# Performance work log

Hardware: AMD Instinct MI355X
Metric: run time of the kernel (lower is better)

The kernel has to match this reference:

```python
import jax, jax.numpy as jnp
import numpy as np

F = 50  # number of feature fields

def setup_inputs() -> dict:
    key = jax.random.key(0)
    k1, k2, k3, k4 = jax.random.split(key, 4)
    B, D, A = 4096, 16, 32
    return {
        "feat_emb": jax.random.normal(k1, (B, F, D), dtype=jnp.float32),
        "W": jax.random.normal(k2, (D, A), dtype=jnp.float32) * 0.1,
        "h": jax.random.normal(k3, (A,), dtype=jnp.float32),
        "p_vec": jax.random.normal(k4, (D,), dtype=jnp.float32),
    }

def reference(feat_emb, W, h, p_vec):
    # build_cross: upper-triangular field pairs (i < j)
    row, col = np.triu_indices(F, k=1)              # each [P], P = F*(F-1)/2
    p = feat_emb[:, row]                             # [B, P, D]
    q = feat_emb[:, col]                             # [B, P, D]
    inter = p * q                                    # pairwise interaction [B, P, D]
    # AttLayer: Dense(no bias) -> relu -> contract with h -> softmax over pairs
    att_signal = jax.nn.relu(jnp.einsum('bpd,da->bpa', inter, W))  # [B, P, A]
    scores = jnp.einsum('bpa,a->bp', att_signal, h)                # [B, P]
    att = jax.nn.softmax(scores, axis=1)                           # [B, P]
    # attention-weighted sum-pooling over pairs
    pooled = jnp.einsum('bp,bpd->bd', att, inter)                  # [B, D]
    # dropout omitted (inference); final projection and reduce
    out = jnp.einsum('bd,d->b', pooled, p_vec)[:, None]            # [B, 1]
    return out
```

## Files before the change

kernel.cpp:

```cpp
#include <hip/hip_runtime.h>
#include <math.h>


#define FF 50
#define DD 16
#define AA 32
#define NP 1225
#define NT 39
#define NTP 40
#define ERS 24
#define EBS (FF * ERS)

typedef _Float16 half8 __attribute__((ext_vector_type(8)));
typedef _Float16 half4 __attribute__((ext_vector_type(4)));
typedef _Float16 half2v __attribute__((ext_vector_type(2)));
typedef float    floatx16 __attribute__((ext_vector_type(16)));

__global__ __launch_bounds__(256, 4) void afm_kernel(
    const float* __restrict__ feat,
    const float* __restrict__ W,
    const float* __restrict__ h,
    const float* __restrict__ pvec,
    float* __restrict__ out,
    int Btot)
{
  __shared__ __align__(16) _Float16 eh[8 * EBS];
  __shared__ unsigned int tbl[NTP * 32];

  const int tid    = threadIdx.x;
  const int lane   = tid & 63;
  const int wave   = tid >> 6;
  const int halfid = lane >> 5;
  const int n      = lane & 31;
  const int b0     = blockIdx.x << 3;

  for (int s = tid; s < 8 * 200; s += 256) {
    int bl  = s / 200;
    int rem = s - bl * 200;
    int bb  = b0 + bl;
    if (bb < Btot) {
      float4 v4 = ((const float4*)feat)[(size_t)bb * 200 + rem];
      half4 hv;
      hv[0] = (_Float16)v4.x; hv[1] = (_Float16)v4.y;
      hv[2] = (_Float16)v4.z; hv[3] = (_Float16)v4.w;
      int row = rem >> 2, q = rem & 3;
      *(half4*)(&eh[bl * EBS + row * ERS + q * 4]) = hv;
    }
  }

  for (int q = tid; q < NTP * 32; q += 256) {
    int t = ((q >> 6) << 1) | (q & 1);
    int nn = (q >> 1) & 31;
    int p = t * 32 + nn;
    unsigned ent = 0;
    if (p < NP) {
      int rad = 9801 - 8 * p;
      int i = (int)((99.0f - sqrtf((float)rad)) * 0.5f);
      if (i < 0) i = 0; if (i > 48) i = 48;
      int off = (i * (99 - i)) >> 1;
      if (off > p) { --i; off = (i * (99 - i)) >> 1; }
      else {
        int off1 = ((i + 1) * (98 - i)) >> 1;
        if (off1 <= p) { ++i; off = off1; }
      }
      int j = p - off + i + 1;
      ent = ((unsigned)(i * 48) << 16) | (unsigned)(j * 48);
    }
    tbl[q] = ent;
  }

  const float LOG2E = 1.4426950408889634f;
  half8 A0;
  #pragma unroll
  for (int jj = 0; jj < 8; ++jj)
    A0[jj] = (_Float16)W[(halfid * 8 + jj) * AA + n];
  float hreg[16];
  #pragma unroll
  for (int r = 0; r < 16; ++r)
    hreg[r] = h[(r & 3) + 8 * (r >> 2) + 4 * halfid] * LOG2E;
  half8 PV;
  #pragma unroll
  for (int k = 0; k < 8; ++k) PV[k] = (_Float16)pvec[halfid * 8 + k];

  __syncthreads();

  const char* ebA = (const char*)(eh + (2 * wave) * EBS) + halfid * 16;
  const char* ebB = ebA + EBS * sizeof(_Float16);

  auto core = [&](const char* eb, unsigned oi, unsigned oj,
                  float& vout, float& gout) {
    half8 Bi = *(const half8*)(eb + oi);
    half8 Bj = *(const half8*)(eb + oj);
    half8 Bv = Bi * Bj;
    floatx16 z = __builtin_amdgcn_mfma_f32_32x32x16_f16(
        A0, Bv, (floatx16)0.0f, 0, 0, 0);
    float a0 = 0.f, a1 = 0.f, a2 = 0.f, a3 = 0.f;
    #pragma unroll
    for (int r = 0; r < 16; r += 4) {
      a0 = fmaf(fmaxf(z[r + 0], 0.f), hreg[r + 0], a0);
      a1 = fmaf(fmaxf(z[r + 1], 0.f), hreg[r + 1], a1);
      a2 = fmaf(fmaxf(z[r + 2], 0.f), hreg[r + 2], a2);
      a3 = fmaf(fmaxf(z[r + 3], 0.f), hreg[r + 3], a3);
    }
    float v = (a0 + a1) + (a2 + a3);
    vout = v + __shfl_xor(v, 32, 64);
    half8 gp = Bv * PV;
    half4 g4 = {(_Float16)(gp[0] + gp[4]), (_Float16)(gp[1] + gp[5]),
                (_Float16)(gp[2] + gp[6]), (_Float16)(gp[3] + gp[7])};
    half2v g2 = {(_Float16)(g4[0] + g4[2]), (_Float16)(g4[1] + g4[3])};
    gout = (float)g2[0] + (float)g2[1];
  };

  float denA = 0.f, numA = 0.f, denB = 0.f, numB = 0.f;

  const unsigned int* tpair = tbl + 2 * n;
  for (int th = 0; th < 19; ++th) {
    uint2 ij2 = *(const uint2*)(tpair + th * 64);
    unsigned oi0 = ij2.x >> 16, oj0 = ij2.x & 0xffffu;
    unsigned oi1 = ij2.y >> 16, oj1 = ij2.y & 0xffffu;
    float v, g;
    core(ebA, oi0, oj0, v, g);
    { float e = exp2f(v); denA += e; numA = fmaf(e, g, numA); }
    core(ebB, oi0, oj0, v, g);
    { float e = exp2f(v); denB += e; numB = fmaf(e, g, numB); }
    core(ebA, oi1, oj1, v, g);
    { float e = exp2f(v); denA += e; numA = fmaf(e, g, numA); }
    core(ebB, oi1, oj1, v, g);
    { float e = exp2f(v); denB += e; numB = fmaf(e, g, numB); }
  }
  {
    unsigned ij = tpair[19 * 64];
    unsigned oi = ij >> 16, oj = ij & 0xffffu;
    float v, g;
    core(ebA, oi, oj, v, g);
    if (n >= 9) v = -3.0e38f;
    { float e = exp2f(v); denA += e; numA = fmaf(e, g, numA); }
    core(ebB, oi, oj, v, g);
    if (n >= 9) v = -3.0e38f;
    { float e = exp2f(v); denB += e; numB = fmaf(e, g, numB); }
  }

  #pragma unroll
  for (int mask = 32; mask >= 1; mask >>= 1) {
    denA += __shfl_xor(denA, mask, 64);
    numA += __shfl_xor(numA, mask, 64);
    denB += __shfl_xor(denB, mask, 64);
    numB += __shfl_xor(numB, mask, 64);
  }
  const int bA = b0 + 2 * wave;
  if (lane == 0 && bA < Btot)     out[bA]     = (2.0f * numA) / denA;
  if (lane == 0 && bA + 1 < Btot) out[bA + 1] = (2.0f * numB) / denB;
}

extern "C" void kernel_launch(void* const* d_in, const int* in_sizes, int n_in,
                              void* d_out, int out_size, void* d_ws, size_t ws_size,
                              hipStream_t stream) {
  const float* feat = (const float*)d_in[0];
  const float* W    = (const float*)d_in[1];
  const float* h    = (const float*)d_in[2];
  const float* pvec = (const float*)d_in[3];
  float* out = (float*)d_out;
  const int B = in_sizes[0] / (FF * DD);
  afm_kernel<<<(B + 7) / 8, 256, 0, stream>>>(feat, W, h, pvec, out, B);
}
```

Before: 89.86 us.

## Process 32 samples per block with 4-sample interleaving per wave

```diff
diff --git a/kernel.cpp b/kernel.cpp
--- a/kernel.cpp
+++ b/kernel.cpp
@@ -10,13 +10,14 @@
 #define NTP 40
 #define ERS 24
 #define EBS (FF * ERS)
+#define BPB 32
 
 typedef _Float16 half8 __attribute__((ext_vector_type(8)));
 typedef _Float16 half4 __attribute__((ext_vector_type(4)));
 typedef _Float16 half2v __attribute__((ext_vector_type(2)));
 typedef float    floatx16 __attribute__((ext_vector_type(16)));
 
-__global__ __launch_bounds__(256, 4) void afm_kernel(
+__global__ __launch_bounds__(256) void afm_kernel(
     const float* __restrict__ feat,
     const float* __restrict__ W,
     const float* __restrict__ h,
@@ -24,7 +25,7 @@
     float* __restrict__ out,
     int Btot)
 {
-  __shared__ __align__(16) _Float16 eh[8 * EBS];
+  __shared__ __align__(16) _Float16 eh[BPB * EBS];
   __shared__ unsigned int tbl[NTP * 32];
 
   const int tid    = threadIdx.x;
@@ -32,9 +33,9 @@
   const int wave   = tid >> 6;
   const int halfid = lane >> 5;
   const int n      = lane & 31;
-  const int b0     = blockIdx.x << 3;
+  const int b0     = blockIdx.x * BPB;
 
-  for (int s = tid; s < 8 * 200; s += 256) {
+  for (int s = tid; s < BPB * 200; s += 256) {
     int bl  = s / 200;
     int rem = s - bl * 200;
     int bb  = b0 + bl;
@@ -81,19 +82,16 @@
   half8 PV;
   #pragma unroll
   for (int k = 0; k < 8; ++k) PV[k] = (_Float16)pvec[halfid * 8 + k];
+  const floatx16 ZACC = (floatx16)0.0f;
 
   __syncthreads();
-
-  const char* ebA = (const char*)(eh + (2 * wave) * EBS) + halfid * 16;
-  const char* ebB = ebA + EBS * sizeof(_Float16);
 
   auto core = [&](const char* eb, unsigned oi, unsigned oj,
                   float& vout, float& gout) {
     half8 Bi = *(const half8*)(eb + oi);
     half8 Bj = *(const half8*)(eb + oj);
     half8 Bv = Bi * Bj;
-    floatx16 z = __builtin_amdgcn_mfma_f32_32x32x16_f16(
-        A0, Bv, (floatx16)0.0f, 0, 0, 0);
+    floatx16 z = __builtin_amdgcn_mfma_f32_32x32x16_f16(A0, Bv, ZACC, 0, 0, 0);
     float a0 = 0.f, a1 = 0.f, a2 = 0.f, a3 = 0.f;
     #pragma unroll
     for (int r = 0; r < 16; r += 4) {
@@ -111,45 +109,61 @@
     gout = (float)g2[0] + (float)g2[1];
   };
 
-  float denA = 0.f, numA = 0.f, denB = 0.f, numB = 0.f;
+  const unsigned int* tpair = tbl + 2 * n;
 
-  const unsigned int* tpair = tbl + 2 * n;
-  for (int th = 0; th < 19; ++th) {
-    uint2 ij2 = *(const uint2*)(tpair + th * 64);
-    unsigned oi0 = ij2.x >> 16, oj0 = ij2.x & 0xffffu;
-    unsigned oi1 = ij2.y >> 16, oj1 = ij2.y & 0xffffu;
-    float v, g;
-    core(ebA, oi0, oj0, v, g);
-    { float e = exp2f(v); denA += e; numA = fmaf(e, g, numA); }
-    core(ebB, oi0, oj0, v, g);
-    { float e = exp2f(v); denB += e; numB = fmaf(e, g, numB); }
-    core(ebA, oi1, oj1, v, g);
-    { float e = exp2f(v); denA += e; numA = fmaf(e, g, numA); }
-    core(ebB, oi1, oj1, v, g);
-    { float e = exp2f(v); denB += e; numB = fmaf(e, g, numB); }
+  for (int grp = 0; grp < 2; ++grp) {
+    const int bg = b0 + wave * 8 + grp * 4;
+    const char* eb0 = (const char*)(eh + (wave * 8 + grp * 4) * EBS)
+                      + halfid * 16;
+    float den[4] = {0.f, 0.f, 0.f, 0.f};
+    float num[4] = {0.f, 0.f, 0.f, 0.f};
+
+    for (int th = 0; th < 19; ++th) {
+      uint2 ij2 = *(const uint2*)(tpair + th * 64);
+      unsigned oi0 = ij2.x >> 16, oj0 = ij2.x & 0xffffu;
+      unsigned oi1 = ij2.y >> 16, oj1 = ij2.y & 0xffffu;
+      #pragma unroll
+      for (int q = 0; q < 4; ++q) {
+        float v, g;
+        core(eb0 + q * (EBS * 2), oi0, oj0, v, g);
+        float e = exp2f(v);
+        den[q] += e; num[q] = fmaf(e, g, num[q]);
+      }
+      #pragma unroll
+      for (int q = 0; q < 4; ++q) {
+        float v, g;
+        core(eb0 + q * (EBS * 2), oi1, oj1, v, g);
+        float e = exp2f(v);
+        den[q] += e; num[q] = fmaf(e, g, num[q]);
+      }
+    }
+    {
+      unsigned ij = tpair[19 * 64];
+      unsigned oi = ij >> 16, oj = ij & 0xffffu;
+      #pragma unroll
+      for (int q = 0; q < 4; ++q) {
+        float v, g;
+        core(eb0 + q * (EBS * 2), oi, oj, v, g);
+        if (n >= 9) v = -3.0e38f;
+        float e = exp2f(v);
+        den[q] += e; num[q] = fmaf(e, g, num[q]);
+      }
+    }
+
+    #pragma unroll
+    for (int mask = 32; mask >= 1; mask >>= 1) {
+      #pragma unroll
+      for (int q = 0; q < 4; ++q) {
+        den[q] += __shfl_xor(den[q], mask, 64);
+        num[q] += __shfl_xor(num[q], mask, 64);
+      }
+    }
+    if (lane == 0) {
+      #pragma unroll
+      for (int q = 0; q < 4; ++q)
+        if (bg + q < Btot) out[bg + q] = (2.0f * num[q]) / den[q];
+    }
   }
-  {
-    unsigned ij = tpair[19 * 64];
-    unsigned oi = ij >> 16, oj = ij & 0xffffu;
-    float v, g;
-    core(ebA, oi, oj, v, g);
-    if (n >= 9) v = -3.0e38f;
-    { float e = exp2f(v); denA += e; numA = fmaf(e, g, numA); }
-    core(ebB, oi, oj, v, g);
-    if (n >= 9) v = -3.0e38f;
-    { float e = exp2f(v); denB += e; numB = fmaf(e, g, numB); }
-  }
-
-  #pragma unroll
-  for (int mask = 32; mask >= 1; mask >>= 1) {
-    denA += __shfl_xor(denA, mask, 64);
-    numA += __shfl_xor(numA, mask, 64);
-    denB += __shfl_xor(denB, mask, 64);
-    numB += __shfl_xor(numB, mask, 64);
-  }
-  const int bA = b0 + 2 * wave;
-  if (lane == 0 && bA < Btot)     out[bA]     = (2.0f * numA) / denA;
-  if (lane == 0 && bA + 1 < Btot) out[bA + 1] = (2.0f * numB) / denB;
 }
 
 extern "C" void kernel_launch(void* const* d_in, const int* in_sizes, int n_in,
@@ -161,5 +175,5 @@
   const float* pvec = (const float*)d_in[3];
   float* out = (float*)d_out;
   const int B = in_sizes[0] / (FF * DD);
-  afm_kernel<<<(B + 7) / 8, 256, 0, stream>>>(feat, W, h, pvec, out, B);
+  afm_kernel<<<(B + BPB - 1) / BPB, 256, 0, stream>>>(feat, W, h, pvec, out, B);
 }
```

New measurement: 144.1 us. 60.3% more time.
